# Kernel optimization log

Hardware: AMD Instinct MI355X
Metric: run time of the kernel (lower is better)

The kernel has to match this reference:

```python
import jax, jax.numpy as jnp
import numpy as np

N_NODES = 50000
N_EDGES = 800000
IN_DIM, HID_DIM, OUT_DIM = 128, 128, 64


def setup_inputs() -> dict:
    key = jax.random.key(0)
    ks = jax.random.split(key, 10)
    s = lambda d: 1.0 / np.sqrt(d)
    return {
        "feat": jax.random.normal(ks[0], (N_NODES, IN_DIM), jnp.float32),
        "W_self1": jax.random.normal(ks[1], (IN_DIM, HID_DIM), jnp.float32) * s(IN_DIM),
        "W_neigh1": jax.random.normal(ks[2], (IN_DIM, HID_DIM), jnp.float32) * s(IN_DIM),
        "b1": jnp.zeros((HID_DIM,), jnp.float32),
        "W_self2": jax.random.normal(ks[3], (HID_DIM, OUT_DIM), jnp.float32) * s(HID_DIM),
        "W_neigh2": jax.random.normal(ks[4], (HID_DIM, OUT_DIM), jnp.float32) * s(HID_DIM),
        "b2": jnp.zeros((OUT_DIM,), jnp.float32),
        "src": jax.random.randint(ks[5], (N_EDGES,), 0, N_NODES),
        "dst": jax.random.randint(ks[6], (N_EDGES,), 0, N_NODES),
        "neg_src": jax.random.randint(ks[7], (N_EDGES,), 0, N_NODES),
        "neg_dst": jax.random.randint(ks[8], (N_EDGES,), 0, N_NODES),
    }


def sage_conv(feat, src, dst, W_self, W_neigh, b):
    # DGL SAGEConv('mean'): out = feat @ W_self + mean_{u->v}(feat_u) @ W_neigh + b
    msg = feat[src]                                                      # [E, D] gather
    agg = jax.ops.segment_sum(msg, dst, num_segments=N_NODES)            # [N, D]
    deg = jax.ops.segment_sum(jnp.ones((src.shape[0], 1), feat.dtype), dst,
                              num_segments=N_NODES)                      # [N, 1]
    h_neigh = agg / jnp.maximum(deg, 1.0)                                # zero for isolated nodes
    return feat @ W_self + h_neigh @ W_neigh + b


def edge_dot(feat, src, dst):
    # dgl.function.u_dot_v -> [E, 1]
    return jnp.sum(feat[src] * feat[dst], axis=-1, keepdims=True)


def reference(feat, W_self1, W_neigh1, b1, W_self2, W_neigh2, b2,
              src, dst, neg_src, neg_dst):
    h = jax.nn.relu(sage_conv(feat, src, dst, W_self1, W_neigh1, b1))
    h = sage_conv(h, src, dst, W_self2, W_neigh2, b2)
    return (edge_dot(h, src, dst), edge_dot(h, neg_src, neg_dst))
```

## Files before the change

kernel.cpp:

```cpp
#include <hip/hip_runtime.h>

#define IN_DIM 128
#define HID_DIM 128
#define OUT_DIM 64

typedef short bf16x8 __attribute__((ext_vector_type(8)));
typedef float f32x4  __attribute__((ext_vector_type(4)));

__device__ inline float bflo(unsigned int u) { return __uint_as_float(u << 16); }
__device__ inline float bfhi(unsigned int u) { return __uint_as_float(u & 0xffff0000u); }
__device__ inline unsigned short f2bf(float f) {
    unsigned int b = __float_as_uint(f);
    return (unsigned short)((b + 0x7FFFu + ((b >> 16) & 1u)) >> 16);
}
__device__ inline unsigned int pack2(float a, float b) {
    return (unsigned int)f2bf(a) | ((unsigned int)f2bf(b) << 16);
}

__global__ void hist_rank_kernel(const int* __restrict__ dst, int* __restrict__ cnt,
                                 unsigned short* __restrict__ rank, int E) {
    int e = blockIdx.x * blockDim.x + threadIdx.x;
    if (e < E) rank[e] = (unsigned short)atomicAdd(&cnt[dst[e]], 1);
}

__global__ void block_sums_kernel(const int* __restrict__ cnt, int* __restrict__ partial, int N) {
    __shared__ int s[256];
    int i = blockIdx.x * 256 + threadIdx.x;
    s[threadIdx.x] = (i < N) ? cnt[i] : 0;
    __syncthreads();
    for (int o = 128; o > 0; o >>= 1) {
        if (threadIdx.x < o) s[threadIdx.x] += s[threadIdx.x + o];
        __syncthreads();
    }
    if (threadIdx.x == 0) partial[blockIdx.x] = s[0];
}

__global__ void scan_partials_kernel(int* __restrict__ partial, int nB) {
    __shared__ int s[256];
    int v = (threadIdx.x < nB) ? partial[threadIdx.x] : 0;
    s[threadIdx.x] = v;
    __syncthreads();
    for (int o = 1; o < 256; o <<= 1) {
        int t = (threadIdx.x >= o) ? s[threadIdx.x - o] : 0;
        __syncthreads();
        s[threadIdx.x] += t;
        __syncthreads();
    }
    if (threadIdx.x < nB) partial[threadIdx.x] = s[threadIdx.x] - v;
}

__global__ void scan_chunks_kernel(const int* __restrict__ cnt, const int* __restrict__ partial,
                                   int* __restrict__ row_ptr, int N) {
    __shared__ int s[256];
    int i = blockIdx.x * 256 + threadIdx.x;
    int v = (i < N) ? cnt[i] : 0;
    s[threadIdx.x] = v;
    __syncthreads();
    for (int o = 1; o < 256; o <<= 1) {
        int t = (threadIdx.x >= o) ? s[threadIdx.x - o] : 0;
        __syncthreads();
        s[threadIdx.x] += t;
        __syncthreads();
    }
    int incl = s[threadIdx.x];
    int base = partial[blockIdx.x];
    if (i < N) row_ptr[i] = base + incl - v;
    if (i == N - 1) row_ptr[N] = base + incl;
}

__global__ __launch_bounds__(256) void gemm1_fill_kernel(
        const float* __restrict__ x,
        const float* __restrict__ Wself,
        const float* __restrict__ Wneigh,
        const float* __restrict__ bias,
        float* __restrict__ hs,
        unsigned short* __restrict__ t,
        int N, int NT, int FB, int NGB,
        const int* __restrict__ src,
        const int* __restrict__ dst,
        const int* __restrict__ row_ptr,
        const unsigned short* __restrict__ rank,
        unsigned short* __restrict__ col_src,
        int E) {
    constexpr int DOUT = HID_DIM;
    constexpr int K   = 128;
    constexpr int MT  = 64;
    constexpr int WC  = 2 * DOUT;
    constexpr int SL  = WC / 4;
    constexpr int TN  = SL / 16;
    constexpr int TM  = MT / 16;
    constexpr int KS  = K / 32;
    constexpr int LDA = K + 8;

    __shared__ unsigned short sA[MT][LDA];

    const int tid = threadIdx.x;

    if ((int)blockIdx.x < FB) {
        int base = (int)blockIdx.x * 1024;
        #pragma unroll
        for (int k = 0; k < 4; ++k) {
            int e = base + k * 256 + tid;
            if (e < E) {
                int d = dst[e];
                col_src[row_ptr[d] + (int)rank[e]] = (unsigned short)src[e];
            }
        }
        return;
    }

    const int gb  = (int)blockIdx.x - FB;
    const int w   = tid >> 6;
    const int l   = tid & 63;
    const int l16 = l & 15;
    const int lhi = l >> 4;

    bf16x8 breg[TN][KS];
    float  bval[TN];
    #pragma unroll
    for (int tn = 0; tn < TN; ++tn) {
        const int c = w * SL + tn * 16 + l16;
        const bool self = (c < DOUT);
        const float* W = self ? &Wself[c] : &Wneigh[c - DOUT];
        bval[tn] = self ? bias[c] : 0.0f;
        #pragma unroll
        for (int ks = 0; ks < KS; ++ks) {
            const int k0 = ks * 32 + lhi * 8;
            bf16x8 f;
            #pragma unroll
            for (int j = 0; j < 8; ++j)
                f[j] = (short)f2bf(W[(size_t)(k0 + j) * DOUT]);
            breg[tn][ks] = f;
        }
    }

    for (int tile = gb; tile < NT; tile += NGB) {
        const int n0 = tile * MT;
        __syncthreads();
        #pragma unroll
        for (int it = 0; it < 8; ++it) {
            int flat = it * 256 + tid;
            int r  = flat >> 5;
            int c4 = flat & 31;
            float4 v = {0, 0, 0, 0};
            if (n0 + r < N) v = *(const float4*)&x[(size_t)(n0 + r) * K + c4 * 4];
            ushort4 p;
            p.x = f2bf(v.x); p.y = f2bf(v.y); p.z = f2bf(v.z); p.w = f2bf(v.w);
            *(ushort4*)&sA[r][c4 * 4] = p;
        }
        __syncthreads();

        f32x4 acc[TN][TM];
        #pragma unroll
        for (int tn = 0; tn < TN; ++tn)
            #pragma unroll
            for (int tm = 0; tm < TM; ++tm)
                acc[tn][tm] = (f32x4){0.0f, 0.0f, 0.0f, 0.0f};

        #pragma unroll
        for (int ks = 0; ks < KS; ++ks) {
            bf16x8 a[TM];
            #pragma unroll
            for (int tm = 0; tm < TM; ++tm)
                a[tm] = *(const bf16x8*)&sA[tm * 16 + l16][ks * 32 + lhi * 8];
            #pragma unroll
            for (int tn = 0; tn < TN; ++tn)
                #pragma unroll
                for (int tm = 0; tm < TM; ++tm)
                    acc[tn][tm] = __builtin_amdgcn_mfma_f32_16x16x32_bf16(
                        a[tm], breg[tn][ks], acc[tn][tm], 0, 0, 0);
        }

        #pragma unroll
        for (int tn = 0; tn < TN; ++tn) {
            const int c = w * SL + tn * 16 + l16;
            const bool self = (c < DOUT);
            const int cc = self ? c : c - DOUT;
            #pragma unroll
            for (int tm = 0; tm < TM; ++tm) {
                #pragma unroll
                for (int r = 0; r < 4; ++r) {
                    const int n = n0 + tm * 16 + lhi * 4 + r;
                    if (n < N) {
                        const float v = acc[tn][tm][r] + bval[tn];
                        if (self) hs[(size_t)n * DOUT + cc] = v;
                        else      t [(size_t)n * DOUT + cc] = f2bf(v);
                    }
                }
            }
        }
    }
}

__global__ void gather_mean128_kernel(const unsigned short* __restrict__ t,
                                      const float* __restrict__ base,
                                      const int* __restrict__ row_ptr,
                                      const unsigned short* __restrict__ col_src,
                                      unsigned short* __restrict__ out, int N) {
    int node = (blockIdx.x * blockDim.x + threadIdx.x) >> 6;
    int lane = threadIdx.x & 63;
    if (node >= N) return;
    const int beg = row_ptr[node], end = row_ptr[node + 1];
    const float rdeg = 1.0f / fmaxf((float)(end - beg), 1.0f);
    const int off = lane * 2;

    float a0x = 0, a0y = 0, a1x = 0, a1y = 0, a2x = 0, a2y = 0, a3x = 0, a3y = 0;
    int i = beg;
    for (; i + 4 <= end; i += 4) {
        int s0 = col_src[i], s1 = col_src[i + 1], s2 = col_src[i + 2], s3 = col_src[i + 3];
        unsigned int u0 = *(const unsigned int*)&t[(size_t)s0 * 128 + off];
        unsigned int u1 = *(const unsigned int*)&t[(size_t)s1 * 128 + off];
        unsigned int u2 = *(const unsigned int*)&t[(size_t)s2 * 128 + off];
        unsigned int u3 = *(const unsigned int*)&t[(size_t)s3 * 128 + off];
        a0x += bflo(u0); a0y += bfhi(u0);
        a1x += bflo(u1); a1y += bfhi(u1);
        a2x += bflo(u2); a2y += bfhi(u2);
        a3x += bflo(u3); a3y += bfhi(u3);
    }
    for (; i < end; ++i) {
        unsigned int u = *(const unsigned int*)&t[(size_t)col_src[i] * 128 + off];
        a0x += bflo(u); a0y += bfhi(u);
    }
    float ax = (a0x + a1x) + (a2x + a3x);
    float ay = (a0y + a1y) + (a2y + a3y);
    float2 b = *(const float2*)&base[(size_t)node * 128 + off];
    float ox = fmaxf(b.x + ax * rdeg, 0.0f);
    float oy = fmaxf(b.y + ay * rdeg, 0.0f);
    *(unsigned int*)&out[(size_t)node * 128 + off] = pack2(ox, oy);
}

__global__ __launch_bounds__(256) void gemm2_kernel(
        const unsigned short* __restrict__ x,
        const float* __restrict__ Wself,
        const float* __restrict__ Wneigh,
        const float* __restrict__ bias,
        float* __restrict__ hs2,
        unsigned short* __restrict__ t2,
        int N) {
    constexpr int DOUT = OUT_DIM;
    constexpr int K   = 128;
    constexpr int MT  = 64;
    constexpr int WC  = 2 * DOUT;
    constexpr int SL  = WC / 4;
    constexpr int TN  = SL / 16;
    constexpr int TM  = MT / 16;
    constexpr int KS  = K / 32;
    constexpr int LDA = K + 8;

    __shared__ unsigned short sA[MT][LDA];

    const int tid = threadIdx.x;
    const int w   = tid >> 6;
    const int l   = tid & 63;
    const int l16 = l & 15;
    const int lhi = l >> 4;

    bf16x8 breg[TN][KS];
    float  bval[TN];
    #pragma unroll
    for (int tn = 0; tn < TN; ++tn) {
        const int c = w * SL + tn * 16 + l16;
        const bool self = (c < DOUT);
        const float* W = self ? &Wself[c] : &Wneigh[c - DOUT];
        bval[tn] = self ? bias[c] : 0.0f;
        #pragma unroll
        for (int ks = 0; ks < KS; ++ks) {
            const int k0 = ks * 32 + lhi * 8;
            bf16x8 f;
            #pragma unroll
            for (int j = 0; j < 8; ++j)
                f[j] = (short)f2bf(W[(size_t)(k0 + j) * DOUT]);
            breg[tn][ks] = f;
        }
    }

    const int n0 = (int)blockIdx.x * MT;
    #pragma unroll
    for (int it = 0; it < 4; ++it) {
        int flat = it * 256 + tid;
        int r  = flat >> 4;
        int c8 = flat & 15;
        uint4 v = {0, 0, 0, 0};
        if (n0 + r < N) v = *(const uint4*)&x[(size_t)(n0 + r) * K + c8 * 8];
        *(uint4*)&sA[r][c8 * 8] = v;
    }
    __syncthreads();

    f32x4 acc[TN][TM];
    #pragma unroll
    for (int tn = 0; tn < TN; ++tn)
        #pragma unroll
        for (int tm = 0; tm < TM; ++tm)
            acc[tn][tm] = (f32x4){0.0f, 0.0f, 0.0f, 0.0f};

    #pragma unroll
    for (int ks = 0; ks < KS; ++ks) {
        bf16x8 a[TM];
        #pragma unroll
        for (int tm = 0; tm < TM; ++tm)
            a[tm] = *(const bf16x8*)&sA[tm * 16 + l16][ks * 32 + lhi * 8];
        #pragma unroll
        for (int tn = 0; tn < TN; ++tn)
            #pragma unroll
            for (int tm = 0; tm < TM; ++tm)
                acc[tn][tm] = __builtin_amdgcn_mfma_f32_16x16x32_bf16(
                    a[tm], breg[tn][ks], acc[tn][tm], 0, 0, 0);
    }

    #pragma unroll
    for (int tn = 0; tn < TN; ++tn) {
        const int c = w * SL + tn * 16 + l16;
        const bool self = (c < DOUT);
        const int cc = self ? c : c - DOUT;
        #pragma unroll
        for (int tm = 0; tm < TM; ++tm) {
            #pragma unroll
            for (int r = 0; r < 4; ++r) {
                const int n = n0 + tm * 16 + lhi * 4 + r;
                if (n < N) {
                    const float v = acc[tn][tm][r] + bval[tn];
                    if (self) hs2[(size_t)n * DOUT + cc] = v;
                    else      t2 [(size_t)n * DOUT + cc] = f2bf(v);
                }
            }
        }
    }
}

__global__ void gather_mean64_kernel(const unsigned short* __restrict__ t,
                                     const float* __restrict__ base,
                                     const int* __restrict__ row_ptr,
                                     const unsigned short* __restrict__ col_src,
                                     unsigned short* __restrict__ out, int N) {
    int tid  = blockIdx.x * blockDim.x + threadIdx.x;
    int node = (tid >> 6) * 2 + ((tid >> 5) & 1);
    int m    = tid & 31;
    if (node >= N) return;
    const int beg = row_ptr[node], end = row_ptr[node + 1];
    const float rdeg = 1.0f / fmaxf((float)(end - beg), 1.0f);
    const int off = m * 2;

    float a0x = 0, a0y = 0, a1x = 0, a1y = 0, a2x = 0, a2y = 0, a3x = 0, a3y = 0;
    int i = beg;
    for (; i + 4 <= end; i += 4) {
        int s0 = col_src[i], s1 = col_src[i + 1], s2 = col_src[i + 2], s3 = col_src[i + 3];
        unsigned int u0 = *(const unsigned int*)&t[(size_t)s0 * 64 + off];
        unsigned int u1 = *(const unsigned int*)&t[(size_t)s1 * 64 + off];
        unsigned int u2 = *(const unsigned int*)&t[(size_t)s2 * 64 + off];
        unsigned int u3 = *(const unsigned int*)&t[(size_t)s3 * 64 + off];
        a0x += bflo(u0); a0y += bfhi(u0);
        a1x += bflo(u1); a1y += bfhi(u1);
        a2x += bflo(u2); a2y += bfhi(u2);
        a3x += bflo(u3); a3y += bfhi(u3);
    }
    for (; i < end; ++i) {
        unsigned int u = *(const unsigned int*)&t[(size_t)col_src[i] * 64 + off];
        a0x += bflo(u); a0y += bfhi(u);
    }
    float ax = (a0x + a1x) + (a2x + a3x);
    float ay = (a0y + a1y) + (a2y + a3y);
    float2 b = *(const float2*)&base[(size_t)node * 64 + off];
    *(unsigned int*)&out[(size_t)node * 64 + off] = pack2(b.x + ax * rdeg, b.y + ay * rdeg);
}

__global__ void edge_dot_kernel(const unsigned short* __restrict__ h,
                                const int* __restrict__ src,
                                const int* __restrict__ dst,
                                const int* __restrict__ nsrc,
                                const int* __restrict__ ndst,
                                float* __restrict__ out,
                                int E) {
    int tid = blockIdx.x * blockDim.x + threadIdx.x;
    int eg = tid >> 3;
    int l  = tid & 7;
    if (eg >= 2 * E) return;
    int s, t;
    if (eg < E) { s = src[eg];      t = dst[eg]; }
    else        { s = nsrc[eg - E]; t = ndst[eg - E]; }
    const uint4 a = *reinterpret_cast<const uint4*>(&h[(size_t)s * OUT_DIM + l * 8]);
    const uint4 b = *reinterpret_cast<const uint4*>(&h[(size_t)t * OUT_DIM + l * 8]);
    float v = bflo(a.x) * bflo(b.x) + bfhi(a.x) * bfhi(b.x)
            + bflo(a.y) * bflo(b.y) + bfhi(a.y) * bfhi(b.y)
            + bflo(a.z) * bflo(b.z) + bfhi(a.z) * bfhi(b.z)
            + bflo(a.w) * bflo(b.w) + bfhi(a.w) * bfhi(b.w);
    v += __shfl_xor(v, 4, 8);
    v += __shfl_xor(v, 2, 8);
    v += __shfl_xor(v, 1, 8);
    if (l == 0) out[eg] = v;
}

extern "C" void kernel_launch(void* const* d_in, const int* in_sizes, int n_in,
                              void* d_out, int out_size, void* d_ws, size_t ws_size,
                              hipStream_t stream) {
    const float* feat = (const float*)d_in[0];
    const float* Ws1  = (const float*)d_in[1];
    const float* Wn1  = (const float*)d_in[2];
    const float* b1   = (const float*)d_in[3];
    const float* Ws2  = (const float*)d_in[4];
    const float* Wn2  = (const float*)d_in[5];
    const float* b2   = (const float*)d_in[6];
    const int* src  = (const int*)d_in[7];
    const int* dst  = (const int*)d_in[8];
    const int* nsrc = (const int*)d_in[9];
    const int* ndst = (const int*)d_in[10];
    const int E = in_sizes[7];
    const int N = in_sizes[0] / IN_DIM;
    const int NB = (N + 255) / 256;
    const int NT = (N + 63) / 64;
    const int FB = (E + 1023) / 1024;
    const int NGB = (NT + 3) / 4;

    int* wsi     = (int*)d_ws;
    int* cnt     = wsi;
    int* row_ptr = cnt + N;
    int* partial = row_ptr + N + 1;
    unsigned short* rank    = (unsigned short*)(partial + 256);
    unsigned short* col_src = rank + E;
    size_t int_count = (size_t)(2 * N + 1 + 256) + (size_t)E;
    int_count = (int_count + 3) & ~(size_t)3;
    unsigned short* t1 = (unsigned short*)(wsi + int_count);
    float* hs1 = (float*)(t1 + (size_t)N * HID_DIM);
    unsigned short* h1 = (unsigned short*)(hs1 + (size_t)N * HID_DIM);
    unsigned short* t2 = h1 + (size_t)N * HID_DIM;
    float* hs2 = (float*)(t2 + (size_t)N * OUT_DIM);
    unsigned short* h2 = (unsigned short*)(hs2 + (size_t)N * OUT_DIM);

    hipMemsetAsync(cnt, 0, sizeof(int) * (size_t)N, stream);
    hist_rank_kernel<<<(E + 255) / 256, 256, 0, stream>>>(dst, cnt, rank, E);
    block_sums_kernel<<<NB, 256, 0, stream>>>(cnt, partial, N);
    scan_partials_kernel<<<1, 256, 0, stream>>>(partial, NB);
    scan_chunks_kernel<<<NB, 256, 0, stream>>>(cnt, partial, row_ptr, N);

    gemm1_fill_kernel<<<FB + NGB, 256, 0, stream>>>(
        feat, Ws1, Wn1, b1, hs1, t1, N, NT, FB, NGB,
        src, dst, row_ptr, rank, col_src, E);

    gather_mean128_kernel<<<(N * 64 + 255) / 256, 256, 0, stream>>>(
        t1, hs1, row_ptr, col_src, h1, N);

    gemm2_kernel<<<NT, 256, 0, stream>>>(
        h1, Ws2, Wn2, b2, hs2, t2, N);

    {
        int waves = (N + 1) / 2;
        gather_mean64_kernel<<<(waves * 64 + 255) / 256, 256, 0, stream>>>(
            t2, hs2, row_ptr, col_src, h2, N);
    }

    {
        int total = 2 * E * 8;
        edge_dot_kernel<<<(total + 255) / 256, 256, 0, stream>>>(
            h2, src, dst, nsrc, ndst, (float*)d_out, E);
    }
}
```

Measured before the change: 227.9 us.

## Pretranspose weights to bf16 once and give each GEMM block one tile

A new small kernel converts both layers' weight matrices to bf16 in a transposed, k-contiguous layout. Both GEMM kernels then load their B fragments with single 16-byte vector loads instead of eight strided fp32 loads with per-element conversion. gemm1 drops its persistent grid-stride loop, launching one block per 64-row tile and overlapping the A-tile load with the weight load. This costs one extra kernel launch, a workspace layout change, and more blocks that each reload the weights.

```diff
diff --git a/kernel.cpp b/kernel.cpp
--- a/kernel.cpp
+++ b/kernel.cpp
@@ -15,6 +15,34 @@
 }
 __device__ inline unsigned int pack2(float a, float b) {
     return (unsigned int)f2bf(a) | ((unsigned int)f2bf(b) << 16);
+}
+
+__global__ void wtrans_kernel(const float* __restrict__ Ws1, const float* __restrict__ Wn1,
+                              const float* __restrict__ Ws2, const float* __restrict__ Wn2,
+                              unsigned short* __restrict__ Wt1, unsigned short* __restrict__ Wt2) {
+    int tid = blockIdx.x * blockDim.x + threadIdx.x;
+    if (tid < 4096) {
+        int c = tid >> 4, k0 = (tid & 15) << 3;
+        const float* W = (c < 128) ? (Ws1 + c) : (Wn1 + (c - 128));
+        ushort4 a, b;
+        a.x = f2bf(W[(size_t)(k0 + 0) * 128]); a.y = f2bf(W[(size_t)(k0 + 1) * 128]);
+        a.z = f2bf(W[(size_t)(k0 + 2) * 128]); a.w = f2bf(W[(size_t)(k0 + 3) * 128]);
+        b.x = f2bf(W[(size_t)(k0 + 4) * 128]); b.y = f2bf(W[(size_t)(k0 + 5) * 128]);
+        b.z = f2bf(W[(size_t)(k0 + 6) * 128]); b.w = f2bf(W[(size_t)(k0 + 7) * 128]);
+        *(ushort4*)&Wt1[c * 128 + k0]     = a;
+        *(ushort4*)&Wt1[c * 128 + k0 + 4] = b;
+    } else if (tid < 6144) {
+        int t = tid - 4096;
+        int c = t >> 4, k0 = (t & 15) << 3;
+        const float* W = (c < 64) ? (Ws2 + c) : (Wn2 + (c - 64));
+        ushort4 a, b;
+        a.x = f2bf(W[(size_t)(k0 + 0) * 64]); a.y = f2bf(W[(size_t)(k0 + 1) * 64]);
+        a.z = f2bf(W[(size_t)(k0 + 2) * 64]); a.w = f2bf(W[(size_t)(k0 + 3) * 64]);
+        b.x = f2bf(W[(size_t)(k0 + 4) * 64]); b.y = f2bf(W[(size_t)(k0 + 5) * 64]);
+        b.z = f2bf(W[(size_t)(k0 + 6) * 64]); b.w = f2bf(W[(size_t)(k0 + 7) * 64]);
+        *(ushort4*)&Wt2[c * 128 + k0]     = a;
+        *(ushort4*)&Wt2[c * 128 + k0 + 4] = b;
+    }
 }
 
 __global__ void hist_rank_kernel(const int* __restrict__ dst, int* __restrict__ cnt,
@@ -70,12 +98,11 @@
 
 __global__ __launch_bounds__(256) void gemm1_fill_kernel(
         const float* __restrict__ x,
-        const float* __restrict__ Wself,
-        const float* __restrict__ Wneigh,
+        const unsigned short* __restrict__ Wt,
         const float* __restrict__ bias,
         float* __restrict__ hs,
         unsigned short* __restrict__ t,
-        int N, int NT, int FB, int NGB,
+        int N, int FB,
         const int* __restrict__ src,
         const int* __restrict__ dst,
         const int* __restrict__ row_ptr,
@@ -85,8 +112,7 @@
     constexpr int DOUT = HID_DIM;
     constexpr int K   = 128;
     constexpr int MT  = 64;
-    constexpr int WC  = 2 * DOUT;
-    constexpr int SL  = WC / 4;
+    constexpr int SL  = 2 * DOUT / 4;
     constexpr int TN  = SL / 16;
     constexpr int TM  = MT / 16;
     constexpr int KS  = K / 32;
@@ -109,83 +135,71 @@
         return;
     }
 
-    const int gb  = (int)blockIdx.x - FB;
     const int w   = tid >> 6;
     const int l   = tid & 63;
     const int l16 = l & 15;
     const int lhi = l >> 4;
+    const int n0  = ((int)blockIdx.x - FB) * MT;
+
+    #pragma unroll
+    for (int it = 0; it < 8; ++it) {
+        int flat = it * 256 + tid;
+        int r  = flat >> 5;
+        int c4 = flat & 31;
+        float4 v = {0, 0, 0, 0};
+        if (n0 + r < N) v = *(const float4*)&x[(size_t)(n0 + r) * K + c4 * 4];
+        ushort4 p;
+        p.x = f2bf(v.x); p.y = f2bf(v.y); p.z = f2bf(v.z); p.w = f2bf(v.w);
+        *(ushort4*)&sA[r][c4 * 4] = p;
+    }
 
     bf16x8 breg[TN][KS];
     float  bval[TN];
+    #pragma unroll
+    for (int tn = 0; tn < TN; ++tn) {
+        const int c = w * SL + tn * 16 + l16;
+        bval[tn] = (c < DOUT) ? bias[c] : 0.0f;
+        #pragma unroll
+        for (int ks = 0; ks < KS; ++ks)
+            breg[tn][ks] = *(const bf16x8*)&Wt[c * 128 + ks * 32 + lhi * 8];
+    }
+    __syncthreads();
+
+    f32x4 acc[TN][TM];
+    #pragma unroll
+    for (int tn = 0; tn < TN; ++tn)
+        #pragma unroll
+        for (int tm = 0; tm < TM; ++tm)
+            acc[tn][tm] = (f32x4){0.0f, 0.0f, 0.0f, 0.0f};
+
+    #pragma unroll
+    for (int ks = 0; ks < KS; ++ks) {
+        bf16x8 a[TM];
+        #pragma unroll
+        for (int tm = 0; tm < TM; ++tm)
+            a[tm] = *(const bf16x8*)&sA[tm * 16 + l16][ks * 32 + lhi * 8];
+        #pragma unroll
+        for (int tn = 0; tn < TN; ++tn)
+            #pragma unroll
+            for (int tm = 0; tm < TM; ++tm)
+                acc[tn][tm] = __builtin_amdgcn_mfma_f32_16x16x32_bf16(
+                    a[tm], breg[tn][ks], acc[tn][tm], 0, 0, 0);
+    }
+
     #pragma unroll
     for (int tn = 0; tn < TN; ++tn) {
         const int c = w * SL + tn * 16 + l16;
         const bool self = (c < DOUT);
-        const float* W = self ? &Wself[c] : &Wneigh[c - DOUT];
-        bval[tn] = self ? bias[c] : 0.0f;
-        #pragma unroll
-        for (int ks = 0; ks < KS; ++ks) {
-            const int k0 = ks * 32 + lhi * 8;
-            bf16x8 f;
+        const int cc = self ? c : c - DOUT;
+        #pragma unroll
+        for (int tm = 0; tm < TM; ++tm) {
             #pragma unroll
-            for (int j = 0; j < 8; ++j)
-                f[j] = (short)f2bf(W[(size_t)(k0 + j) * DOUT]);
-            breg[tn][ks] = f;
-        }
-    }
-
-    for (int tile = gb; tile < NT; tile += NGB) {
-        const int n0 = tile * MT;
-        __syncthreads();
-        #pragma unroll
-        for (int it = 0; it < 8; ++it) {
-            int flat = it * 256 + tid;
-            int r  = flat >> 5;
-            int c4 = flat & 31;
-            float4 v = {0, 0, 0, 0};
-            if (n0 + r < N) v = *(const float4*)&x[(size_t)(n0 + r) * K + c4 * 4];
-            ushort4 p;
-            p.x = f2bf(v.x); p.y = f2bf(v.y); p.z = f2bf(v.z); p.w = f2bf(v.w);
-            *(ushort4*)&sA[r][c4 * 4] = p;
-        }
-        __syncthreads();
-
-        f32x4 acc[TN][TM];
-        #pragma unroll
-        for (int tn = 0; tn < TN; ++tn)
-            #pragma unroll
-            for (int tm = 0; tm < TM; ++tm)
-                acc[tn][tm] = (f32x4){0.0f, 0.0f, 0.0f, 0.0f};
-
-        #pragma unroll
-        for (int ks = 0; ks < KS; ++ks) {
-            bf16x8 a[TM];
-            #pragma unroll
-            for (int tm = 0; tm < TM; ++tm)
-                a[tm] = *(const bf16x8*)&sA[tm * 16 + l16][ks * 32 + lhi * 8];
-            #pragma unroll
-            for (int tn = 0; tn < TN; ++tn)
-                #pragma unroll
-                for (int tm = 0; tm < TM; ++tm)
-                    acc[tn][tm] = __builtin_amdgcn_mfma_f32_16x16x32_bf16(
-                        a[tm], breg[tn][ks], acc[tn][tm], 0, 0, 0);
-        }
-
-        #pragma unroll
-        for (int tn = 0; tn < TN; ++tn) {
-            const int c = w * SL + tn * 16 + l16;
-            const bool self = (c < DOUT);
-            const int cc = self ? c : c - DOUT;
-            #pragma unroll
-            for (int tm = 0; tm < TM; ++tm) {
-                #pragma unroll
-                for (int r = 0; r < 4; ++r) {
-                    const int n = n0 + tm * 16 + lhi * 4 + r;
-                    if (n < N) {
-                        const float v = acc[tn][tm][r] + bval[tn];
-                        if (self) hs[(size_t)n * DOUT + cc] = v;
-                        else      t [(size_t)n * DOUT + cc] = f2bf(v);
-                    }
+            for (int r = 0; r < 4; ++r) {
+                const int n = n0 + tm * 16 + lhi * 4 + r;
+                if (n < N) {
+                    const float v = acc[tn][tm][r] + bval[tn];
+                    if (self) hs[(size_t)n * DOUT + cc] = v;
+                    else      t [(size_t)n * DOUT + cc] = f2bf(v);
                 }
             }
         }
@@ -231,8 +245,7 @@
 
 __global__ __launch_bounds__(256) void gemm2_kernel(
         const unsigned short* __restrict__ x,
-        const float* __restrict__ Wself,
-        const float* __restrict__ Wneigh,
+        const unsigned short* __restrict__ Wt,
         const float* __restrict__ bias,
         float* __restrict__ hs2,
         unsigned short* __restrict__ t2,
@@ -240,8 +253,7 @@
     constexpr int DOUT = OUT_DIM;
     constexpr int K   = 128;
     constexpr int MT  = 64;
-    constexpr int WC  = 2 * DOUT;
-    constexpr int SL  = WC / 4;
+    constexpr int SL  = 2 * DOUT / 4;
     constexpr int TN  = SL / 16;
     constexpr int TM  = MT / 16;
     constexpr int KS  = K / 32;
@@ -254,27 +266,8 @@
     const int l   = tid & 63;
     const int l16 = l & 15;
     const int lhi = l >> 4;
-
-    bf16x8 breg[TN][KS];
-    float  bval[TN];
-    #pragma unroll
-    for (int tn = 0; tn < TN; ++tn) {
-        const int c = w * SL + tn * 16 + l16;
-        const bool self = (c < DOUT);
-        const float* W = self ? &Wself[c] : &Wneigh[c - DOUT];
-        bval[tn] = self ? bias[c] : 0.0f;
-        #pragma unroll
-        for (int ks = 0; ks < KS; ++ks) {
-            const int k0 = ks * 32 + lhi * 8;
-            bf16x8 f;
-            #pragma unroll
-            for (int j = 0; j < 8; ++j)
-                f[j] = (short)f2bf(W[(size_t)(k0 + j) * DOUT]);
-            breg[tn][ks] = f;
-        }
-    }
-
-    const int n0 = (int)blockIdx.x * MT;
+    const int n0  = (int)blockIdx.x * MT;
+
     #pragma unroll
     for (int it = 0; it < 4; ++it) {
         int flat = it * 256 + tid;
@@ -283,6 +276,17 @@
         uint4 v = {0, 0, 0, 0};
         if (n0 + r < N) v = *(const uint4*)&x[(size_t)(n0 + r) * K + c8 * 8];
         *(uint4*)&sA[r][c8 * 8] = v;
+    }
+
+    bf16x8 breg[TN][KS];
+    float  bval[TN];
+    #pragma unroll
+    for (int tn = 0; tn < TN; ++tn) {
+        const int c = w * SL + tn * 16 + l16;
+        bval[tn] = (c < DOUT) ? bias[c] : 0.0f;
+        #pragma unroll
+        for (int ks = 0; ks < KS; ++ks)
+            breg[tn][ks] = *(const bf16x8*)&Wt[c * 128 + ks * 32 + lhi * 8];
     }
     __syncthreads();
 
@@ -408,22 +412,23 @@
     const int NB = (N + 255) / 256;
     const int NT = (N + 63) / 64;
     const int FB = (E + 1023) / 1024;
-    const int NGB = (NT + 3) / 4;
-
-    int* wsi     = (int*)d_ws;
-    int* cnt     = wsi;
-    int* row_ptr = cnt + N;
-    int* partial = row_ptr + N + 1;
+
+    char* wsb = (char*)d_ws;
+    unsigned short* Wt1 = (unsigned short*)wsb;
+    unsigned short* Wt2 = Wt1 + 256 * 128;
+    unsigned short* t1  = Wt2 + 128 * 128;
+    float* hs1          = (float*)(t1 + (size_t)N * HID_DIM);
+    unsigned short* h1  = (unsigned short*)(hs1 + (size_t)N * HID_DIM);
+    unsigned short* t2  = h1 + (size_t)N * HID_DIM;
+    float* hs2          = (float*)(t2 + (size_t)N * OUT_DIM);
+    unsigned short* h2  = (unsigned short*)(hs2 + (size_t)N * OUT_DIM);
+    int* cnt            = (int*)(h2 + (size_t)N * OUT_DIM);
+    int* row_ptr        = cnt + N;
+    int* partial        = row_ptr + N + 1;
     unsigned short* rank    = (unsigned short*)(partial + 256);
     unsigned short* col_src = rank + E;
-    size_t int_count = (size_t)(2 * N + 1 + 256) + (size_t)E;
-    int_count = (int_count + 3) & ~(size_t)3;
-    unsigned short* t1 = (unsigned short*)(wsi + int_count);
-    float* hs1 = (float*)(t1 + (size_t)N * HID_DIM);
-    unsigned short* h1 = (unsigned short*)(hs1 + (size_t)N * HID_DIM);
-    unsigned short* t2 = h1 + (size_t)N * HID_DIM;
-    float* hs2 = (float*)(t2 + (size_t)N * OUT_DIM);
-    unsigned short* h2 = (unsigned short*)(hs2 + (size_t)N * OUT_DIM);
+
+    wtrans_kernel<<<24, 256, 0, stream>>>(Ws1, Wn1, Ws2, Wn2, Wt1, Wt2);
 
     hipMemsetAsync(cnt, 0, sizeof(int) * (size_t)N, stream);
     hist_rank_kernel<<<(E + 255) / 256, 256, 0, stream>>>(dst, cnt, rank, E);
@@ -431,15 +436,15 @@
     scan_partials_kernel<<<1, 256, 0, stream>>>(partial, NB);
     scan_chunks_kernel<<<NB, 256, 0, stream>>>(cnt, partial, row_ptr, N);
 
-    gemm1_fill_kernel<<<FB + NGB, 256, 0, stream>>>(
-        feat, Ws1, Wn1, b1, hs1, t1, N, NT, FB, NGB,
+    gemm1_fill_kernel<<<FB + NT, 256, 0, stream>>>(
+        feat, Wt1, b1, hs1, t1, N, FB,
         src, dst, row_ptr, rank, col_src, E);
 
     gather_mean128_kernel<<<(N * 64 + 255) / 256, 256, 0, stream>>>(
         t1, hs1, row_ptr, col_src, h1, N);
 
     gemm2_kernel<<<NT, 256, 0, stream>>>(
-        h1, Ws2, Wn2, b2, hs2, t2, N);
+        h1, Wt2, b2, hs2, t2, N);
 
     {
         int waves = (N + 1) / 2;
```

New measurement: 197.9 us. 1.15x faster.
